# Performance work log

Measured on AMD Instinct MI355X. Metric: run time of the kernel, lower is better.

The kernel has to match this reference:

```python
import jax, jax.numpy as jnp
import numpy as np

B, N, CIN, H, D, K = 8, 1000, 16, 64, 16, 3  # batch, nodes, in_dim, hidden, embed_dim, cheb_k
XIN = CIN + H  # GRU concat input dim


def setup_inputs() -> dict:
    key = jax.random.key(0)
    ks = jax.random.split(key, 18)
    f = lambda k, s, sc=1.0: jax.random.normal(k, s, dtype=jnp.float32) * sc
    inp = {}
    inp['x1'] = f(ks[0], (B, N, CIN)); inp['x2'] = f(ks[1], (B, N, CIN)); inp['x3'] = f(ks[2], (B, N, CIN))
    inp['state1'] = f(ks[3], (B, N, H)); inp['state2'] = f(ks[4], (B, N, H)); inp['state3'] = f(ks[5], (B, N, H))
    for i, name in enumerate(['support1', 'support2', 'support3']):
        a = jax.random.uniform(ks[6 + i], (N, N), dtype=jnp.float32)
        inp[name] = a / a.sum(-1, keepdims=True)  # row-stochastic graph, keeps Chebyshev stable
    inp['embeddings1'] = f(ks[9], (N, D), 0.1); inp['embeddings2'] = f(ks[10], (N, D), 0.1); inp['embeddings3'] = f(ks[11], (N, D), 0.1)
    inp['mode_embedding'] = f(ks[12], (3, D), 0.5)
    # xavier-normal-ish scales for the hypernet weight pools
    inp['Wg'] = f(ks[13], (D, K * XIN, 2 * H), (2.0 / (K * XIN * 2 * H + D * 2 * H)) ** 0.5)
    inp['Bg'] = f(ks[14], (D, 2 * H), (2.0 / (D + 2 * H)) ** 0.5)
    inp['Wu'] = f(ks[15], (D, K * XIN, H), (2.0 / (K * XIN * H + D * H)) ** 0.5)
    inp['Bu'] = f(ks[16], (D, H), (2.0 / (D + H)) ** 0.5)
    return inp


def _cheb_gcn(x, support, emb, wp, bp):
    # x:[B,N,C], support:[N,N], emb:[N,D], wp:[D,K*C,O], bp:[D,O]
    # Chebyshev recurrence applied directly to features (equivalent to building T_k(support))
    terms = [x, jnp.einsum('nm,bmc->bnc', support, x)]
    for _ in range(2, K):
        terms.append(2.0 * jnp.einsum('nm,bmc->bnc', support, terms[-1]) - terms[-2])
    x_g = jnp.concatenate(terms, axis=-1)  # [B,N,K*C]
    # meta_axis='S': per-node weights = emb @ wp ; fused contraction
    out = jnp.einsum('bni,nd,dio->bno', x_g, emb, wp) + emb @ bp  # [B,N,O]
    return out


def _cell(x, state, support, emb, me, Wg, Bg, Wu, Bu):
    # me:[D] mode embedding scales the shared pools (einsum 'mc,cdf->mcdf' -> pick mode m)
    zr = jax.nn.sigmoid(_cheb_gcn(jnp.concatenate([x, state], -1), support, emb,
                                  me[:, None, None] * Wg, me[:, None] * Bg))
    z, r = jnp.split(zr, 2, axis=-1)
    hc = jnp.tanh(_cheb_gcn(jnp.concatenate([x, z * state], -1), support, emb,
                            me[:, None, None] * Wu, me[:, None] * Bu))
    return r * state + (1.0 - r) * hc


def reference(x1, x2, x3, state1, state2, state3, support1, support2, support3,
              embeddings1, embeddings2, embeddings3, mode_embedding, Wg, Bg, Wu, Bu):
    h1 = _cell(x1, state1, support1, embeddings1, mode_embedding[0], Wg, Bg, Wu, Bu)
    h2 = _cell(x2, state2, support2, embeddings2, mode_embedding[1], Wg, Bg, Wu, Bu)
    h3 = _cell(x3, state3, support3, embeddings3, mode_embedding[2], Wg, Bg, Wu, Bu)
    return (h1, h2, h3)
```

## Files before the change

kernel.cpp:

```cpp
#include <hip/hip_runtime.h>
#include <math.h>


typedef __attribute__((ext_vector_type(8))) short s16x8;
typedef __attribute__((ext_vector_type(4))) float f32x4;
typedef unsigned short u16;
typedef unsigned int u32;
typedef unsigned long long u64;

__device__ __forceinline__ u32 f2bf(float f) {
  union { float f; u32 u; } v; v.f = f;
  return (v.u + 0x7FFFu + ((v.u >> 16) & 1u)) >> 16;
}
__device__ __forceinline__ float bf2f(u16 h) {
  union { u32 u; float f; } v; v.u = (u32)h << 16; return v.f;
}
__device__ __forceinline__ void glds16(const u16* g, u16* l) {
  __builtin_amdgcn_global_load_lds(
      (const __attribute__((address_space(1))) void*)g,
      (__attribute__((address_space(3))) void*)l, 16, 0, 0);
}

#define E0 3145728
#define E1 1966080
#define E2 1920000
#define E3 384000
#define E4 384000
#define E5 384000
#define E6 119808

struct PrepArgs {
  const float* x[3]; const float* st[3]; const float* S[3];
  u16 *S16, *Xt, *Ag, *AgU, *T1t, *ZSt, *SZ1t;
};

__global__ void prep(PrepArgs P) {
  long idx = (long)blockIdx.x * 256 + threadIdx.x;
  if (idx < E0) {
    int m = (int)(idx >> 20); int rem = (int)(idx & 1048575);
    int n = rem >> 10, k = rem & 1023;
    float v = (n < 1000 && k < 1000) ? P.S[m][n * 1000 + k] : 0.f;
    P.S16[(size_t)m * 1048576 + rem] = (u16)f2bf(v); return;
  }
  idx -= E0;
  if (idx < E1) {
    int m = (int)(idx / 655360); int rem = (int)(idx % 655360);
    int col = rem >> 10, nn = rem & 1023;
    int b = col / 80, c = col % 80;
    float v = 0.f;
    if (nn < 1000) v = (c < 16) ? P.x[m][(b * 1000 + nn) * 16 + c]
                                : P.st[m][(b * 1000 + nn) * 64 + c - 16];
    P.Xt[(size_t)m * 655360 + rem] = (u16)f2bf(v); return;
  }
  idx -= E1;
  if (idx < E2) {
    int m = (int)(idx / 640000); int rem = (int)(idx % 640000);
    int r = rem / 80, c = rem % 80;
    int n = r >> 3, b = r & 7;
    float v = (c < 16) ? P.x[m][(b * 1000 + n) * 16 + c]
                       : P.st[m][(b * 1000 + n) * 64 + c - 16];
    P.Ag[(size_t)m * 2048000 + (size_t)r * 256 + c] = (u16)f2bf(v); return;
  }
  idx -= E2;
  if (idx < E3) {
    int m = (int)(idx / 128000); int rem = (int)(idx % 128000);
    int r = rem / 16, c = 240 + rem % 16;
    P.Ag[(size_t)m * 2048000 + (size_t)r * 256 + c] = 0; return;
  }
  idx -= E3;
  if (idx < E4) {
    int m = (int)(idx / 128000); int rem = (int)(idx % 128000);
    int r = rem / 16, c = rem % 16;
    int n = r >> 3, b = r & 7;
    P.AgU[(size_t)m * 2048000 + (size_t)r * 256 + c] =
        (u16)f2bf(P.x[m][(b * 1000 + n) * 16 + c]); return;
  }
  idx -= E4;
  if (idx < E5) {
    int m = (int)(idx / 128000); int rem = (int)(idx % 128000);
    int r = rem / 16, c = 240 + rem % 16;
    P.AgU[(size_t)m * 2048000 + (size_t)r * 256 + c] = 0; return;
  }
  idx -= E5;
  if (idx < E6) {
    int m = (int)(idx / 39936); int rem = (int)(idx % 39936);
    if (rem < 15360) { int col = rem / 24, j = rem % 24;
      P.T1t[(size_t)m * 655360 + col * 1024 + 1000 + j] = 0; }
    else if (rem < 27648) { int e = rem - 15360; int col = e / 24, j = e % 24;
      P.ZSt[(size_t)m * 524288 + col * 1024 + 1000 + j] = 0; }
    else { int e = rem - 27648; int col = e / 24, j = e % 24;
      P.SZ1t[(size_t)m * 524288 + col * 1024 + 1000 + j] = 0; }
    return;
  }
}

__global__ void bias_kernel(const float* __restrict__ e0, const float* __restrict__ e1,
                            const float* __restrict__ e2, const float* __restrict__ me,
                            const float* __restrict__ Bp, int O, float* __restrict__ outB) {
  int idx = blockIdx.x * blockDim.x + threadIdx.x;
  int total = 3 * 1000 * O;
  if (idx >= total) return;
  int mode = idx / (1000 * O);
  int rem  = idx % (1000 * O);
  int n = rem / O, o = rem % O;
  const float* emb = (mode == 0) ? e0 : (mode == 1) ? e1 : e2;
  float s = 0.f;
#pragma unroll
  for (int d = 0; d < 16; ++d)
    s += emb[n * 16 + d] * me[mode * 16 + d] * Bp[d * O + o];
  outB[idx] = s;
}

__global__ void packW_kernel(const float* __restrict__ Wg, const float* __restrict__ Wu,
                             u16* __restrict__ BtG, u16* __restrict__ BtU) {
  int idx = blockIdx.x * blockDim.x + threadIdx.x;
  if (idx >= (2048 + 1024) * 256) return;
  if (idx < 2048 * 256) {
    int col = idx >> 8, k = idx & 255;
    int d = col >> 7, o = col & 127;
    BtG[idx] = (k < 240) ? (u16)f2bf(Wg[d * 30720 + k * 128 + o]) : (u16)0;
  } else {
    int i2 = idx - 2048 * 256;
    int col = i2 >> 8, k = i2 & 255;
    int d = col >> 6, o = col & 63;
    BtU[i2] = (k < 240) ? (u16)f2bf(Wu[d * 15360 + k * 64 + o]) : (u16)0;
  }
}

struct ChebArgs2 {
  const u16* S16[3]; const u16* A[3]; const u16* Res[3];
  u16* Yt[3]; u16* AgA[3]; u16* AgX[3];
};

__global__ __launch_bounds__(256, 2) void cheb_v4(ChebArgs2 g, int fdiv, int agbase,
                                                  float alpha, float beta, int flags) {
  const int mode = blockIdx.z;
  const u16* __restrict__ Ab = g.A[mode];
  const u16* __restrict__ Sb = g.S16[mode];

  __shared__ u16 As[64 * 64];
  __shared__ u16 Bs[64 * 64];

  const int t = threadIdx.x;
  const int row0 = blockIdx.y * 64, n0 = blockIdx.x * 64;
  const int lane = t & 63, wid = t >> 6;
  const int l16 = lane & 15, quad = lane >> 4;
  const int wy = (wid >> 1) * 32, wx = (wid & 1) * 32;

  f32x4 acc[2][2];
#pragma unroll
  for (int a = 0; a < 2; ++a)
#pragma unroll
    for (int b = 0; b < 2; ++b) acc[a][b] = (f32x4){0.f, 0.f, 0.f, 0.f};

  for (int k0 = 0; k0 < 1024; k0 += 64) {
#pragma unroll
    for (int p = 0; p < 2; ++p) {
      int idx = p * 256 + t; int row = idx >> 3; int cs = (idx & 7) ^ (row & 7);
      glds16(Ab + (size_t)(row0 + row) * 1024 + k0 + cs * 8, &As[idx * 8]);
    }
#pragma unroll
    for (int p = 0; p < 2; ++p) {
      int idx = p * 256 + t; int row = idx >> 3; int cs = (idx & 7) ^ (row & 7);
      glds16(Sb + (size_t)(n0 + row) * 1024 + k0 + cs * 8, &Bs[idx * 8]);
    }
    __syncthreads();
    s16x8 af[2][2], bf[2][2];
#pragma unroll
    for (int mi = 0; mi < 2; ++mi) {
      int row = wy + mi * 16 + l16;
#pragma unroll
      for (int ks = 0; ks < 2; ++ks) {
        int cl = (ks * 4 + quad) ^ (row & 7);
        af[mi][ks] = *(const s16x8*)&As[row * 64 + cl * 8];
      }
    }
#pragma unroll
    for (int ni = 0; ni < 2; ++ni) {
      int row = wx + ni * 16 + l16;
#pragma unroll
      for (int ks = 0; ks < 2; ++ks) {
        int cl = (ks * 4 + quad) ^ (row & 7);
        bf[ni][ks] = *(const s16x8*)&Bs[row * 64 + cl * 8];
      }
    }
#pragma unroll
    for (int ks = 0; ks < 2; ++ks)
#pragma unroll
      for (int mi = 0; mi < 2; ++mi)
#pragma unroll
        for (int ni = 0; ni < 2; ++ni)
          acc[mi][ni] = __builtin_amdgcn_mfma_f32_16x16x32_bf16(af[mi][ks], bf[ni][ks], acc[mi][ni], 0, 0, 0);
    __syncthreads();
  }

#pragma unroll
  for (int mi = 0; mi < 2; ++mi) {
    int frow0 = row0 + wy + mi * 16 + quad * 4;
    int b = frow0 / fdiv, c0 = frow0 - b * fdiv;
#pragma unroll
    for (int ni = 0; ni < 2; ++ni) {
      int n = n0 + wx + ni * 16 + l16;
      if (n < 1000) {
        u16 pk[4];
#pragma unroll
        for (int r = 0; r < 4; ++r) {
          float v = alpha * acc[mi][ni][r];
          if (flags & 1) v += beta * bf2f(g.Res[mode][(size_t)(frow0 + r) * 1024 + n]);
          u16 h = (u16)f2bf(v);
          pk[r] = h;
          if (flags & 2) g.Yt[mode][(size_t)(frow0 + r) * 1024 + n] = h;
        }
        u64 pv = (u64)pk[0] | ((u64)pk[1] << 16) | ((u64)pk[2] << 32) | ((u64)pk[3] << 48);
        *(u64*)&g.AgA[mode][(size_t)(n * 8 + b) * 256 + agbase + c0] = pv;
        if ((flags & 4) && c0 < 16)
          *(u64*)&g.AgX[mode][(size_t)(n * 8 + b) * 256 + agbase + c0] = pv;
      }
    }
  }
}

struct Meta3Args {
  const u16* Ag;
  const u16* Bt;
  const float* emb[3];
  const float* me;
  const float* Bias;
  const float* state[3];
  u16* ZSt;
  u16* AgU;
  float* Rb;
  float* out;
};

__global__ __launch_bounds__(256, 2) void meta3(Meta3Args A, int is_gate, int O) {
  const int mode = blockIdx.z;
  const int row0 = blockIdx.y * 64;
  const int n0 = row0 >> 3;

  __shared__ u16 As[64 * 256];
  __shared__ u16 Bs[64 * 256];
  __shared__ float ewS[8][17];

  const int t = threadIdx.x;
  if (t < 128) {
    int nl = t >> 4, d = t & 15;
    ewS[nl][d] = A.emb[mode][(n0 + nl) * 16 + d] * A.me[mode * 16 + d];
  }

  const int lane = t & 63, wid = t >> 6;
  const int l16 = lane & 15, quad = lane >> 4;
  const int wy = (wid >> 1) * 32, wx = (wid & 1) * 32;
  const u16* Agm = A.Ag + (size_t)mode * 2048000;

#pragma unroll
  for (int p = 0; p < 8; ++p) {
    int idx = p * 256 + t; int row = idx >> 5; int cs = (idx & 31) ^ (row & 7);
    glds16(Agm + (size_t)(row0 + row) * 256 + cs * 8, &As[idx * 8]);
  }
  __syncthreads();

  s16x8 afr[2][8];
#pragma unroll
  for (int mi = 0; mi < 2; ++mi) {
    int row = wy + mi * 16 + l16;
#pragma unroll
    for (int ki = 0; ki < 8; ++ki) {
      int cl = (ki * 4 + quad) ^ (row & 7);
      afr[mi][ki] = *(const s16x8*)&As[row * 256 + cl * 8];
    }
  }

  f32x4 outacc[2][2][2];
#pragma unroll
  for (int a = 0; a < 2; ++a)
#pragma unroll
    for (int b = 0; b < 2; ++b)
#pragma unroll
      for (int c = 0; c < 2; ++c) outacc[a][b][c] = (f32x4){0.f, 0.f, 0.f, 0.f};

  const int shift = (O == 128) ? 1 : 0;
  const int ntiles = O >> 2;

  for (int tl = 0; tl < ntiles; ++tl) {
    const int d = tl >> shift;
    const int oc = tl & shift;
    __syncthreads();
    const int brow0 = d * O + oc * 64;
#pragma unroll
    for (int p = 0; p < 8; ++p) {
      int idx = p * 256 + t; int row = idx >> 5; int cs = (idx & 31) ^ (row & 7);
      glds16(A.Bt + (size_t)(brow0 + row) * 256 + cs * 8, &Bs[idx * 8]);
    }
    __syncthreads();

    f32x4 acc[2][2];
#pragma unroll
    for (int a = 0; a < 2; ++a)
#pragma unroll
      for (int b = 0; b < 2; ++b) acc[a][b] = (f32x4){0.f, 0.f, 0.f, 0.f};

#pragma unroll
    for (int ki = 0; ki < 8; ++ki) {
      s16x8 bfr[2];
#pragma unroll
      for (int ni = 0; ni < 2; ++ni) {
        int row = wx + ni * 16 + l16;
        int cl = (ki * 4 + quad) ^ (row & 7);
        bfr[ni] = *(const s16x8*)&Bs[row * 256 + cl * 8];
      }
#pragma unroll
      for (int mi = 0; mi < 2; ++mi)
#pragma unroll
        for (int ni = 0; ni < 2; ++ni)
          acc[mi][ni] = __builtin_amdgcn_mfma_f32_16x16x32_bf16(afr[mi][ki], bfr[ni], acc[mi][ni], 0, 0, 0);
    }

#pragma unroll
    for (int mi = 0; mi < 2; ++mi) {
      int nl = (wy + mi * 16 + quad * 4) >> 3;
      float s = ewS[nl][d];
#pragma unroll
      for (int ni = 0; ni < 2; ++ni)
#pragma unroll
        for (int r = 0; r < 4; ++r)
          outacc[oc][mi][ni][r] += s * acc[mi][ni][r];
    }
  }

#pragma unroll
  for (int oc = 0; oc <= shift; ++oc)
#pragma unroll
    for (int mi = 0; mi < 2; ++mi)
#pragma unroll
      for (int ni = 0; ni < 2; ++ni)
#pragma unroll
        for (int r = 0; r < 4; ++r) {
          int row = row0 + wy + mi * 16 + quad * 4 + r;
          int n = row >> 3, b = row & 7;
          int o = oc * 64 + wx + ni * 16 + l16;
          float pre = outacc[oc][mi][ni][r] + A.Bias[(size_t)mode * 1000 * O + n * O + o];
          if (is_gate) {
            float sg = 1.f / (1.f + __expf(-pre));
            if (o < 64) {
              float st = A.state[mode][(b * 1000 + n) * 64 + o];
              float zs = sg * st;
              A.ZSt[(size_t)mode * 524288 + (size_t)(b * 64 + o) * 1024 + n] = (u16)f2bf(zs);
              A.AgU[(size_t)mode * 2048000 + (size_t)row * 256 + 16 + o] = (u16)f2bf(zs);
            } else {
              A.Rb[(size_t)mode * 512000 + row * 64 + (o - 64)] = sg;
            }
          } else {
            float hc = tanhf(pre);
            float rr = A.Rb[(size_t)mode * 512000 + row * 64 + o];
            float st = A.state[mode][(b * 1000 + n) * 64 + o];
            A.out[(size_t)mode * 512000 + (b * 1000 + n) * 64 + o] = rr * st + (1.f - rr) * hc;
          }
        }
}

extern "C" void kernel_launch(void* const* d_in, const int* in_sizes, int n_in,
                              void* d_out, int out_size, void* d_ws, size_t ws_size,
                              hipStream_t stream) {
  const float* x[3]   = {(const float*)d_in[0], (const float*)d_in[1], (const float*)d_in[2]};
  const float* st[3]  = {(const float*)d_in[3], (const float*)d_in[4], (const float*)d_in[5]};
  const float* S[3]   = {(const float*)d_in[6], (const float*)d_in[7], (const float*)d_in[8]};
  const float* emb[3] = {(const float*)d_in[9], (const float*)d_in[10], (const float*)d_in[11]};
  const float* me = (const float*)d_in[12];
  const float* Wg = (const float*)d_in[13];
  const float* Bg = (const float*)d_in[14];
  const float* Wu = (const float*)d_in[15];
  const float* Bu = (const float*)d_in[16];
  float* out = (float*)d_out;

  float* BiG = (float*)d_ws;
  float* BiU = BiG + 384000;
  float* Rb  = BiU + 192000;
  u16* S16 = (u16*)(Rb + 1536000);
  u16* Xt  = S16 + 3145728;
  u16* T1t = Xt + 1966080;
  u16* ZSt = T1t + 1966080;
  u16* SZ1t= ZSt + 1572864;
  u16* Ag  = SZ1t + 1572864;
  u16* AgU = Ag + 6144000;
  u16* BtG = AgU + 6144000;
  u16* BtU = BtG + 524288;

  {
    PrepArgs P;
    for (int m = 0; m < 3; ++m) { P.x[m] = x[m]; P.st[m] = st[m]; P.S[m] = S[m]; }
    P.S16 = S16; P.Xt = Xt; P.Ag = Ag; P.AgU = AgU; P.T1t = T1t; P.ZSt = ZSt; P.SZ1t = SZ1t;
    prep<<<32436, 256, 0, stream>>>(P);
  }
  bias_kernel<<<1500, 256, 0, stream>>>(emb[0], emb[1], emb[2], me, Bg, 128, BiG);
  bias_kernel<<<750, 256, 0, stream>>>(emb[0], emb[1], emb[2], me, Bu, 64, BiU);
  packW_kernel<<<3072, 256, 0, stream>>>(Wg, Wu, BtG, BtU);

  {
    ChebArgs2 a;
    for (int m = 0; m < 3; ++m) {
      a.S16[m] = S16 + (size_t)m * 1048576; a.A[m] = Xt + (size_t)m * 655360;
      a.Res[m] = nullptr; a.Yt[m] = T1t + (size_t)m * 655360;
      a.AgA[m] = Ag + (size_t)m * 2048000; a.AgX[m] = AgU + (size_t)m * 2048000;
    }
    cheb_v4<<<dim3(16, 10, 3), 256, 0, stream>>>(a, 80, 80, 1.f, 0.f, 2 | 4);
  }
  {
    ChebArgs2 a;
    for (int m = 0; m < 3; ++m) {
      a.S16[m] = S16 + (size_t)m * 1048576; a.A[m] = T1t + (size_t)m * 655360;
      a.Res[m] = Xt + (size_t)m * 655360; a.Yt[m] = nullptr;
      a.AgA[m] = Ag + (size_t)m * 2048000; a.AgX[m] = AgU + (size_t)m * 2048000;
    }
    cheb_v4<<<dim3(16, 10, 3), 256, 0, stream>>>(a, 80, 160, 2.f, -1.f, 1 | 4);
  }
  {
    Meta3Args a;
    a.Ag = Ag; a.Bt = BtG; a.me = me; a.Bias = BiG;
    a.ZSt = ZSt; a.AgU = AgU; a.Rb = Rb; a.out = out;
    for (int m = 0; m < 3; ++m) { a.emb[m] = emb[m]; a.state[m] = st[m]; }
    meta3<<<dim3(1, 125, 3), 256, 0, stream>>>(a, 1, 128);
  }
  {
    ChebArgs2 a;
    for (int m = 0; m < 3; ++m) {
      a.S16[m] = S16 + (size_t)m * 1048576; a.A[m] = ZSt + (size_t)m * 524288;
      a.Res[m] = nullptr; a.Yt[m] = SZ1t + (size_t)m * 524288;
      a.AgA[m] = AgU + (size_t)m * 2048000; a.AgX[m] = nullptr;
    }
    cheb_v4<<<dim3(16, 8, 3), 256, 0, stream>>>(a, 64, 96, 1.f, 0.f, 2);
  }
  {
    ChebArgs2 a;
    for (int m = 0; m < 3; ++m) {
      a.S16[m] = S16 + (size_t)m * 1048576; a.A[m] = SZ1t + (size_t)m * 524288;
      a.Res[m] = ZSt + (size_t)m * 524288; a.Yt[m] = nullptr;
      a.AgA[m] = AgU + (size_t)m * 2048000; a.AgX[m] = nullptr;
    }
    cheb_v4<<<dim3(16, 8, 3), 256, 0, stream>>>(a, 64, 176, 2.f, -1.f, 1);
  }
  {
    Meta3Args a;
    a.Ag = AgU; a.Bt = BtU; a.me = me; a.Bias = BiU;
    a.ZSt = ZSt; a.AgU = AgU; a.Rb = Rb; a.out = out;
    for (int m = 0; m < 3; ++m) { a.emb[m] = emb[m]; a.state[m] = st[m]; }
    meta3<<<dim3(1, 125, 3), 256, 0, stream>>>(a, 0, 64);
  }
}
```

Before: 273.0 us.

## Double-buffer B tiles in meta3 and split output halves across blocks

```diff
diff --git a/kernel.cpp b/kernel.cpp
--- a/kernel.cpp
+++ b/kernel.cpp
@@ -237,6 +237,8 @@
   const int mode = blockIdx.z;
   const int row0 = blockIdx.y * 64;
   const int n0 = row0 >> 3;
+  const int oc = blockIdx.x;
+  const int ocbase = oc * 64;
 
   __shared__ u16 As[64 * 256];
   __shared__ u16 Bs[64 * 256];
@@ -253,12 +255,26 @@
   const int wy = (wid >> 1) * 32, wx = (wid & 1) * 32;
   const u16* Agm = A.Ag + (size_t)mode * 2048000;
 
+#define STAGE_B(TL, BUF)                                                      \
+  {                                                                           \
+    const int brow0_ = (TL) * O + ocbase;                                     \
+    _Pragma("unroll")                                                         \
+    for (int p_ = 0; p_ < 8; ++p_) {                                          \
+      int idx_ = p_ * 256 + t; int row_ = idx_ >> 5;                          \
+      int cs_ = (idx_ & 31) ^ (row_ & 7);                                     \
+      glds16(A.Bt + (size_t)(brow0_ + row_) * 256 + cs_ * 8, &(BUF)[idx_ * 8]); \
+    }                                                                         \
+  }
+
 #pragma unroll
   for (int p = 0; p < 8; ++p) {
     int idx = p * 256 + t; int row = idx >> 5; int cs = (idx & 31) ^ (row & 7);
     glds16(Agm + (size_t)(row0 + row) * 256 + cs * 8, &As[idx * 8]);
   }
-  __syncthreads();
+  STAGE_B(0, Bs);
+
+  asm volatile("s_waitcnt vmcnt(8) lgkmcnt(0)" ::: "memory");
+  __builtin_amdgcn_s_barrier();
 
   s16x8 afr[2][8];
 #pragma unroll
@@ -270,29 +286,21 @@
       afr[mi][ki] = *(const s16x8*)&As[row * 256 + cl * 8];
     }
   }
-
-  f32x4 outacc[2][2][2];
+  asm volatile("s_waitcnt lgkmcnt(0)" ::: "memory");
+  __builtin_amdgcn_s_barrier();
+  STAGE_B(1, As);
+
+  f32x4 outacc[2][2];
 #pragma unroll
   for (int a = 0; a < 2; ++a)
 #pragma unroll
-    for (int b = 0; b < 2; ++b)
-#pragma unroll
-      for (int c = 0; c < 2; ++c) outacc[a][b][c] = (f32x4){0.f, 0.f, 0.f, 0.f};
-
-  const int shift = (O == 128) ? 1 : 0;
-  const int ntiles = O >> 2;
-
-  for (int tl = 0; tl < ntiles; ++tl) {
-    const int d = tl >> shift;
-    const int oc = tl & shift;
-    __syncthreads();
-    const int brow0 = d * O + oc * 64;
-#pragma unroll
-    for (int p = 0; p < 8; ++p) {
-      int idx = p * 256 + t; int row = idx >> 5; int cs = (idx & 31) ^ (row & 7);
-      glds16(A.Bt + (size_t)(brow0 + row) * 256 + cs * 8, &Bs[idx * 8]);
-    }
-    __syncthreads();
+    for (int b = 0; b < 2; ++b) outacc[a][b] = (f32x4){0.f, 0.f, 0.f, 0.f};
+
+  for (int tl = 0; tl < 16; ++tl) {
+    u16* buf = (tl & 1) ? As : Bs;
+    if (tl < 15) asm volatile("s_waitcnt vmcnt(8)" ::: "memory");
+    else         asm volatile("s_waitcnt vmcnt(0)" ::: "memory");
+    __builtin_amdgcn_s_barrier();
 
     f32x4 acc[2][2];
 #pragma unroll
@@ -307,7 +315,7 @@
       for (int ni = 0; ni < 2; ++ni) {
         int row = wx + ni * 16 + l16;
         int cl = (ki * 4 + quad) ^ (row & 7);
-        bfr[ni] = *(const s16x8*)&Bs[row * 256 + cl * 8];
+        bfr[ni] = *(const s16x8*)&buf[row * 256 + cl * 8];
       }
 #pragma unroll
       for (int mi = 0; mi < 2; ++mi)
@@ -319,44 +327,47 @@
 #pragma unroll
     for (int mi = 0; mi < 2; ++mi) {
       int nl = (wy + mi * 16 + quad * 4) >> 3;
-      float s = ewS[nl][d];
+      float s = ewS[nl][tl];
 #pragma unroll
       for (int ni = 0; ni < 2; ++ni)
 #pragma unroll
         for (int r = 0; r < 4; ++r)
-          outacc[oc][mi][ni][r] += s * acc[mi][ni][r];
-    }
-  }
-
-#pragma unroll
-  for (int oc = 0; oc <= shift; ++oc)
-#pragma unroll
-    for (int mi = 0; mi < 2; ++mi)
-#pragma unroll
-      for (int ni = 0; ni < 2; ++ni)
-#pragma unroll
-        for (int r = 0; r < 4; ++r) {
-          int row = row0 + wy + mi * 16 + quad * 4 + r;
-          int n = row >> 3, b = row & 7;
-          int o = oc * 64 + wx + ni * 16 + l16;
-          float pre = outacc[oc][mi][ni][r] + A.Bias[(size_t)mode * 1000 * O + n * O + o];
-          if (is_gate) {
-            float sg = 1.f / (1.f + __expf(-pre));
-            if (o < 64) {
-              float st = A.state[mode][(b * 1000 + n) * 64 + o];
-              float zs = sg * st;
-              A.ZSt[(size_t)mode * 524288 + (size_t)(b * 64 + o) * 1024 + n] = (u16)f2bf(zs);
-              A.AgU[(size_t)mode * 2048000 + (size_t)row * 256 + 16 + o] = (u16)f2bf(zs);
-            } else {
-              A.Rb[(size_t)mode * 512000 + row * 64 + (o - 64)] = sg;
-            }
+          outacc[mi][ni][r] += s * acc[mi][ni][r];
+    }
+
+    asm volatile("s_waitcnt lgkmcnt(0)" ::: "memory");
+    __builtin_amdgcn_s_barrier();
+    if (tl + 2 < 16) STAGE_B(tl + 2, buf);
+  }
+#undef STAGE_B
+
+#pragma unroll
+  for (int mi = 0; mi < 2; ++mi)
+#pragma unroll
+    for (int ni = 0; ni < 2; ++ni)
+#pragma unroll
+      for (int r = 0; r < 4; ++r) {
+        int row = row0 + wy + mi * 16 + quad * 4 + r;
+        int n = row >> 3, b = row & 7;
+        int o = ocbase + wx + ni * 16 + l16;
+        float pre = outacc[mi][ni][r] + A.Bias[(size_t)mode * 1000 * O + n * O + o];
+        if (is_gate) {
+          float sg = 1.f / (1.f + __expf(-pre));
+          if (o < 64) {
+            float st = A.state[mode][(b * 1000 + n) * 64 + o];
+            float zs = sg * st;
+            A.ZSt[(size_t)mode * 524288 + (size_t)(b * 64 + o) * 1024 + n] = (u16)f2bf(zs);
+            A.AgU[(size_t)mode * 2048000 + (size_t)row * 256 + 16 + o] = (u16)f2bf(zs);
           } else {
-            float hc = tanhf(pre);
-            float rr = A.Rb[(size_t)mode * 512000 + row * 64 + o];
-            float st = A.state[mode][(b * 1000 + n) * 64 + o];
-            A.out[(size_t)mode * 512000 + (b * 1000 + n) * 64 + o] = rr * st + (1.f - rr) * hc;
+            A.Rb[(size_t)mode * 512000 + row * 64 + (o - 64)] = sg;
           }
+        } else {
+          float hc = tanhf(pre);
+          float rr = A.Rb[(size_t)mode * 512000 + row * 64 + o];
+          float st = A.state[mode][(b * 1000 + n) * 64 + o];
+          A.out[(size_t)mode * 512000 + (b * 1000 + n) * 64 + o] = rr * st + (1.f - rr) * hc;
         }
+      }
 }
 
 extern "C" void kernel_launch(void* const* d_in, const int* in_sizes, int n_in,
@@ -419,7 +430,7 @@
     a.Ag = Ag; a.Bt = BtG; a.me = me; a.Bias = BiG;
     a.ZSt = ZSt; a.AgU = AgU; a.Rb = Rb; a.out = out;
     for (int m = 0; m < 3; ++m) { a.emb[m] = emb[m]; a.state[m] = st[m]; }
-    meta3<<<dim3(1, 125, 3), 256, 0, stream>>>(a, 1, 128);
+    meta3<<<dim3(2, 125, 3), 256, 0, stream>>>(a, 1, 128);
   }
   {
     ChebArgs2 a;
```

After: 279.6 us. 1.02x slower.

## Split meta3 output columns across blocks and reuse LDS buffer for A tile

Applied to the files above, without the earlier changes.

```diff
diff --git a/kernel.cpp b/kernel.cpp
--- a/kernel.cpp
+++ b/kernel.cpp
@@ -233,12 +233,13 @@
   float* out;
 };
 
-__global__ __launch_bounds__(256, 2) void meta3(Meta3Args A, int is_gate, int O) {
+__global__ __launch_bounds__(256, 4) void meta3(Meta3Args A, int is_gate, int O) {
   const int mode = blockIdx.z;
   const int row0 = blockIdx.y * 64;
   const int n0 = row0 >> 3;
-
-  __shared__ u16 As[64 * 256];
+  const int oc = blockIdx.x;
+  const int ocbase = oc * 64;
+
   __shared__ u16 Bs[64 * 256];
   __shared__ float ewS[8][17];
 
@@ -256,7 +257,7 @@
 #pragma unroll
   for (int p = 0; p < 8; ++p) {
     int idx = p * 256 + t; int row = idx >> 5; int cs = (idx & 31) ^ (row & 7);
-    glds16(Agm + (size_t)(row0 + row) * 256 + cs * 8, &As[idx * 8]);
+    glds16(Agm + (size_t)(row0 + row) * 256 + cs * 8, &Bs[idx * 8]);
   }
   __syncthreads();
 
@@ -267,26 +268,19 @@
 #pragma unroll
     for (int ki = 0; ki < 8; ++ki) {
       int cl = (ki * 4 + quad) ^ (row & 7);
-      afr[mi][ki] = *(const s16x8*)&As[row * 256 + cl * 8];
-    }
-  }
-
-  f32x4 outacc[2][2][2];
+      afr[mi][ki] = *(const s16x8*)&Bs[row * 256 + cl * 8];
+    }
+  }
+  __syncthreads();
+
+  f32x4 outacc[2][2];
 #pragma unroll
   for (int a = 0; a < 2; ++a)
 #pragma unroll
-    for (int b = 0; b < 2; ++b)
-#pragma unroll
-      for (int c = 0; c < 2; ++c) outacc[a][b][c] = (f32x4){0.f, 0.f, 0.f, 0.f};
-
-  const int shift = (O == 128) ? 1 : 0;
-  const int ntiles = O >> 2;
-
-  for (int tl = 0; tl < ntiles; ++tl) {
-    const int d = tl >> shift;
-    const int oc = tl & shift;
-    __syncthreads();
-    const int brow0 = d * O + oc * 64;
+    for (int b = 0; b < 2; ++b) outacc[a][b] = (f32x4){0.f, 0.f, 0.f, 0.f};
+
+  for (int tl = 0; tl < 16; ++tl) {
+    const int brow0 = tl * O + ocbase;
 #pragma unroll
     for (int p = 0; p < 8; ++p) {
       int idx = p * 256 + t; int row = idx >> 5; int cs = (idx & 31) ^ (row & 7);
@@ -319,44 +313,43 @@
 #pragma unroll
     for (int mi = 0; mi < 2; ++mi) {
       int nl = (wy + mi * 16 + quad * 4) >> 3;
-      float s = ewS[nl][d];
+      float s = ewS[nl][tl];
 #pragma unroll
       for (int ni = 0; ni < 2; ++ni)
 #pragma unroll
         for (int r = 0; r < 4; ++r)
-          outacc[oc][mi][ni][r] += s * acc[mi][ni][r];
-    }
-  }
-
-#pragma unroll
-  for (int oc = 0; oc <= shift; ++oc)
-#pragma unroll
-    for (int mi = 0; mi < 2; ++mi)
-#pragma unroll
-      for (int ni = 0; ni < 2; ++ni)
-#pragma unroll
-        for (int r = 0; r < 4; ++r) {
-          int row = row0 + wy + mi * 16 + quad * 4 + r;
-          int n = row >> 3, b = row & 7;
-          int o = oc * 64 + wx + ni * 16 + l16;
-          float pre = outacc[oc][mi][ni][r] + A.Bias[(size_t)mode * 1000 * O + n * O + o];
-          if (is_gate) {
-            float sg = 1.f / (1.f + __expf(-pre));
-            if (o < 64) {
-              float st = A.state[mode][(b * 1000 + n) * 64 + o];
-              float zs = sg * st;
-              A.ZSt[(size_t)mode * 524288 + (size_t)(b * 64 + o) * 1024 + n] = (u16)f2bf(zs);
-              A.AgU[(size_t)mode * 2048000 + (size_t)row * 256 + 16 + o] = (u16)f2bf(zs);
-            } else {
-              A.Rb[(size_t)mode * 512000 + row * 64 + (o - 64)] = sg;
-            }
+          outacc[mi][ni][r] += s * acc[mi][ni][r];
+    }
+    __syncthreads();
+  }
+
+#pragma unroll
+  for (int mi = 0; mi < 2; ++mi)
+#pragma unroll
+    for (int ni = 0; ni < 2; ++ni)
+#pragma unroll
+      for (int r = 0; r < 4; ++r) {
+        int row = row0 + wy + mi * 16 + quad * 4 + r;
+        int n = row >> 3, b = row & 7;
+        int o = ocbase + wx + ni * 16 + l16;
+        float pre = outacc[mi][ni][r] + A.Bias[(size_t)mode * 1000 * O + n * O + o];
+        if (is_gate) {
+          float sg = 1.f / (1.f + __expf(-pre));
+          if (o < 64) {
+            float st = A.state[mode][(b * 1000 + n) * 64 + o];
+            float zs = sg * st;
+            A.ZSt[(size_t)mode * 524288 + (size_t)(b * 64 + o) * 1024 + n] = (u16)f2bf(zs);
+            A.AgU[(size_t)mode * 2048000 + (size_t)row * 256 + 16 + o] = (u16)f2bf(zs);
           } else {
-            float hc = tanhf(pre);
-            float rr = A.Rb[(size_t)mode * 512000 + row * 64 + o];
-            float st = A.state[mode][(b * 1000 + n) * 64 + o];
-            A.out[(size_t)mode * 512000 + (b * 1000 + n) * 64 + o] = rr * st + (1.f - rr) * hc;
+            A.Rb[(size_t)mode * 512000 + row * 64 + (o - 64)] = sg;
           }
+        } else {
+          float hc = tanhf(pre);
+          float rr = A.Rb[(size_t)mode * 512000 + row * 64 + o];
+          float st = A.state[mode][(b * 1000 + n) * 64 + o];
+          A.out[(size_t)mode * 512000 + (b * 1000 + n) * 64 + o] = rr * st + (1.f - rr) * hc;
         }
+      }
 }
 
 extern "C" void kernel_launch(void* const* d_in, const int* in_sizes, int n_in,
@@ -419,7 +412,7 @@
     a.Ag = Ag; a.Bt = BtG; a.me = me; a.Bias = BiG;
     a.ZSt = ZSt; a.AgU = AgU; a.Rb = Rb; a.out = out;
     for (int m = 0; m < 3; ++m) { a.emb[m] = emb[m]; a.state[m] = st[m]; }
-    meta3<<<dim3(1, 125, 3), 256, 0, stream>>>(a, 1, 128);
+    meta3<<<dim3(2, 125, 3), 256, 0, stream>>>(a, 1, 128);
   }
   {
     ChebArgs2 a;
```

Result: no change. 271.7 us (-0.5%).
